# Kernel optimization log

Measured on AMD Instinct MI355X. Metric: run time of the kernel, lower is better.

## Reference

```python
import jax, jax.numpy as jnp
import numpy as np

N_NEWS, N_ENT, N_TOP = 100000, 50000, 2000
D = 128
N_EDGES = 1600000
HID, OUT = 512, 128


def setup_inputs() -> dict:
    key = jax.random.key(0)
    ks = jax.random.split(key, 12)
    return {
        "news_feats": jax.random.normal(ks[0], (N_NEWS, D), jnp.float32),
        "entity_feats": jax.random.normal(ks[1], (N_ENT, D), jnp.float32),
        "topic_feats": jax.random.normal(ks[2], (N_TOP, D), jnp.float32),
        "ent_row": jax.random.randint(ks[3], (N_EDGES,), 0, N_NEWS, jnp.int32),
        "ent_col": jax.random.randint(ks[4], (N_EDGES,), 0, N_ENT, jnp.int32),
        "top_row": jax.random.randint(ks[5], (N_EDGES,), 0, N_NEWS, jnp.int32),
        "top_col": jax.random.randint(ks[6], (N_EDGES,), 0, N_TOP, jnp.int32),
        "W1": jax.random.normal(ks[7], (3 * D, HID), jnp.float32) * 0.05,
        "b1": jnp.zeros((HID,), jnp.float32),
        "W2": jax.random.normal(ks[8], (HID, OUT), jnp.float32) * 0.05,
        "b2": jnp.zeros((OUT,), jnp.float32),
    }


def _agg(feats, row, col, num_news):
    # SpMM with binary adjacency: sum neighbor feats per news node
    gathered = feats[col]                                   # [E, D]
    summed = jax.ops.segment_sum(gathered, row, num_segments=num_news)
    deg = jax.ops.segment_sum(jnp.ones_like(row, dtype=feats.dtype), row,
                              num_segments=num_news)
    return summed / (deg[:, None] + 1e-8)


def reference(news_feats, entity_feats, topic_feats, ent_row, ent_col,
              top_row, top_col, W1, b1, W2, b2):
    n = news_feats.shape[0]
    ent_agg = _agg(entity_feats, ent_row, ent_col, n)
    top_agg = _agg(topic_feats, top_row, top_col, n)
    out = jnp.concatenate([news_feats, ent_agg, top_agg], axis=1)  # [N, 3D]
    h = jnp.tanh(out @ W1 + b1)
    return h @ W2 + b2
```

## Files before the change

### kernel.cpp

```cpp
#include <hip/hip_runtime.h>
#include <hip/hip_bf16.h>

#define NN 100000
#define NE 50000
#define NT 2000
#define DD 128
#define NEDGE 1600000
#define HID 512
#define OUTD 128
#define K1 (3*DD)
#define NBKT 391
#define ECAP 4608

typedef __bf16 bf16x8 __attribute__((ext_vector_type(8)));
typedef __bf16 bf16x4 __attribute__((ext_vector_type(4)));
typedef float  f32x4  __attribute__((ext_vector_type(4)));

__device__ __forceinline__ __bf16 f2b(float f) {
    __hip_bfloat16 h = __float2bfloat16(f);
    union { __hip_bfloat16 h; __bf16 b; } u; u.h = h; return u.b;
}

__device__ __forceinline__ void gll16(const void* g, void* l) {
    __builtin_amdgcn_global_load_lds((const __attribute__((address_space(1))) void*)g,
                                     (__attribute__((address_space(3))) void*)l, 16, 0, 0);
}

__device__ __forceinline__ float ftanh(float x) {
    x = fminf(fmaxf(x, -15.f), 15.f);
    float t = __expf(2.f * x);
    return (t - 1.f) / (t + 1.f);
}

__global__ void conv_feats(const float* __restrict__ entf, const float* __restrict__ topf,
                           const float* __restrict__ news,
                           __bf16* __restrict__ entb, __bf16* __restrict__ topb,
                           __bf16* __restrict__ X) {
    long i = ((long)blockIdx.x * 256 + threadIdx.x) * 4;
    const long NEL = (long)NE * DD;
    const long NTL = (long)NT * DD;
    if (i < NEL) {
        float4 v = *(const float4*)(entf + i);
        *(bf16x4*)(entb + i) = bf16x4{f2b(v.x), f2b(v.y), f2b(v.z), f2b(v.w)};
    } else if (i < NEL + NTL) {
        long j = i - NEL;
        float4 v = *(const float4*)(topf + j);
        *(bf16x4*)(topb + j) = bf16x4{f2b(v.x), f2b(v.y), f2b(v.z), f2b(v.w)};
    } else {
        long j = i - NEL - NTL;
        long row = j >> 7, col = j & 127;
        float4 v = *(const float4*)(news + j);
        *(bf16x4*)(X + row * K1 + col) = bf16x4{f2b(v.x), f2b(v.y), f2b(v.z), f2b(v.w)};
    }
}

__global__ __launch_bounds__(256) void scatter_bucket(const int* __restrict__ er,
                                                      const int* __restrict__ ec,
                                                      const int* __restrict__ tr,
                                                      const int* __restrict__ tc,
                                                      int* __restrict__ cnt_e,
                                                      int* __restrict__ cnt_t,
                                                      int* __restrict__ be,
                                                      int* __restrict__ bt) {
    __shared__ int lhe[NBKT], lht[NBKT];
    __shared__ int lbe[NBKT], lbt[NBKT];
    const int tid = threadIdx.x;
    for (int i = tid; i < NBKT; i += 256) { lhe[i] = 0; lht[i] = 0; }
    __syncthreads();
    const int base = blockIdx.x * 4096;
    #pragma unroll 4
    for (int k = 0; k < 16; k++) {
        int e = base + k * 256 + tid;
        if (e < NEDGE) {
            atomicAdd(&lhe[er[e] >> 8], 1);
            atomicAdd(&lht[tr[e] >> 8], 1);
        }
    }
    __syncthreads();
    for (int i = tid; i < NBKT; i += 256) {
        int c = lhe[i];
        lbe[i] = c ? (i * ECAP + atomicAdd(&cnt_e[i], c)) : 0;
        lhe[i] = 0;
        c = lht[i];
        lbt[i] = c ? (i * ECAP + atomicAdd(&cnt_t[i], c)) : 0;
        lht[i] = 0;
    }
    __syncthreads();
    #pragma unroll 4
    for (int k = 0; k < 16; k++) {
        int e = base + k * 256 + tid;
        if (e < NEDGE) {
            int r = er[e];
            int b = r >> 8;
            int p = lbe[b] + atomicAdd(&lhe[b], 1);
            be[p] = ((r & 255) << 16) | ec[e];
            r = tr[e];
            b = r >> 8;
            p = lbt[b] + atomicAdd(&lht[b], 1);
            bt[p] = ((r & 255) << 16) | tc[e];
        }
    }
}

__global__ __launch_bounds__(256) void bucket_csr(const int* __restrict__ be,
                                                  const int* __restrict__ bt,
                                                  const int* __restrict__ cnt_e,
                                                  const int* __restrict__ cnt_t,
                                                  int* __restrict__ starts_e,
                                                  int* __restrict__ ends_e,
                                                  int* __restrict__ starts_t,
                                                  int* __restrict__ ends_t,
                                                  int* __restrict__ se,
                                                  int* __restrict__ st) {
    const int* buf  = blockIdx.y ? bt : be;
    const int* bcnt = blockIdx.y ? cnt_t : cnt_e;
    int* starts     = blockIdx.y ? starts_t : starts_e;
    int* ends       = blockIdx.y ? ends_t : ends_e;
    int* sout       = blockIdx.y ? st : se;
    const int b = blockIdx.x;
    const int tid = threadIdx.x;
    const int start = b * ECAP;
    int cnt = bcnt[b]; if (cnt > ECAP) cnt = ECAP;

    __shared__ int scn[256];
    __shared__ int lcur[256];
    scn[tid] = 0;
    __syncthreads();
    for (int i = tid; i < cnt; i += 256)
        atomicAdd(&scn[buf[start + i] >> 16], 1);
    __syncthreads();
    #pragma unroll
    for (int off = 1; off < 256; off <<= 1) {
        int v = (tid >= off) ? scn[tid - off] : 0;
        __syncthreads();
        scn[tid] += v;
        __syncthreads();
    }
    const int node = b * 256 + tid;
    const int excl = start + (tid ? scn[tid - 1] : 0);
    if (node < NN) {
        starts[node] = excl;
        ends[node]   = start + scn[tid];
    }
    lcur[tid] = excl;
    __syncthreads();
    for (int i = tid; i < cnt; i += 256) {
        int v = buf[start + i];
        int p = atomicAdd(&lcur[v >> 16], 1);
        sout[p] = v & 0xFFFF;
    }
}

__global__ __launch_bounds__(256) void aggregate2(const __bf16* __restrict__ entb,
                                                  const __bf16* __restrict__ topb,
                                                  const int* __restrict__ starts_e,
                                                  const int* __restrict__ ends_e,
                                                  const int* __restrict__ starts_t,
                                                  const int* __restrict__ ends_t,
                                                  const int* __restrict__ se,
                                                  const int* __restrict__ st,
                                                  __bf16* __restrict__ X) {
    __shared__ int sidx[4][128];
    const int wave = threadIdx.x >> 6, lane = threadIdx.x & 63;
    const int node = blockIdx.x * 4 + wave;
    if (node >= NN) return;
    const int g = lane >> 4;
    const int d = (lane & 15) * 8;

    const int s0 = starts_e[node], s1 = ends_e[node];
    const int t0 = starts_t[node], t1 = ends_t[node];
    const int dege = s1 - s0, degt = t1 - t0;
    const int lim_e = dege < 64 ? dege : 64;
    const int lim_t = degt < 64 ? degt : 64;

    int* my = sidx[wave];
    if (lane < lim_e) my[lane] = se[s0 + lane];
    if (lane < lim_t) my[64 + lane] = st[t0 + lane];

    float ea[8] = {0,0,0,0,0,0,0,0};
    float pa[8] = {0,0,0,0,0,0,0,0};

    const int lim = lim_e > lim_t ? lim_e : lim_t;
    for (int e = g; e < lim; e += 4) {
        if (e < lim_e) {
            bf16x8 v = *(const bf16x8*)(entb + (long)my[e] * DD + d);
            #pragma unroll
            for (int j = 0; j < 8; j++) ea[j] += (float)v[j];
        }
        if (e < lim_t) {
            bf16x8 v = *(const bf16x8*)(topb + (long)my[64 + e] * DD + d);
            #pragma unroll
            for (int j = 0; j < 8; j++) pa[j] += (float)v[j];
        }
    }
    for (int e = 64 + g; e < dege; e += 4) {
        bf16x8 v = *(const bf16x8*)(entb + (long)se[s0 + e] * DD + d);
        #pragma unroll
        for (int j = 0; j < 8; j++) ea[j] += (float)v[j];
    }
    for (int e = 64 + g; e < degt; e += 4) {
        bf16x8 v = *(const bf16x8*)(topb + (long)st[t0 + e] * DD + d);
        #pragma unroll
        for (int j = 0; j < 8; j++) pa[j] += (float)v[j];
    }

    #pragma unroll
    for (int j = 0; j < 8; j++) {
        ea[j] += __shfl_xor(ea[j], 16, 64);
        ea[j] += __shfl_xor(ea[j], 32, 64);
        pa[j] += __shfl_xor(pa[j], 16, 64);
        pa[j] += __shfl_xor(pa[j], 32, 64);
    }

    const float ie = 1.0f / ((float)dege + 1e-8f);
    const float it = 1.0f / ((float)degt + 1e-8f);
    __bf16* xr = X + (long)node * K1;
    if (g == 1) {
        *(bf16x8*)(xr + DD + d) = bf16x8{f2b(ea[0]*ie), f2b(ea[1]*ie), f2b(ea[2]*ie), f2b(ea[3]*ie),
                                         f2b(ea[4]*ie), f2b(ea[5]*ie), f2b(ea[6]*ie), f2b(ea[7]*ie)};
    } else if (g == 2) {
        *(bf16x8*)(xr + 2*DD + d) = bf16x8{f2b(pa[0]*it), f2b(pa[1]*it), f2b(pa[2]*it), f2b(pa[3]*it),
                                           f2b(pa[4]*it), f2b(pa[5]*it), f2b(pa[6]*it), f2b(pa[7]*it)};
    }
}

__global__ void conv_w(const float* __restrict__ W1, const float* __restrict__ W2,
                       __bf16* __restrict__ W1T, __bf16* __restrict__ W2T) {
    int i = blockIdx.x * 256 + threadIdx.x;
    if (i < K1 * HID) {
        int k = i / HID, n = i % HID;
        W1T[n * K1 + k] = f2b(W1[i]);
    } else {
        int j = i - K1 * HID;
        if (j < HID * OUTD) {
            int k = j / OUTD, n = j % OUTD;
            W2T[n * HID + k] = f2b(W2[j]);
        }
    }
}


__device__ __forceinline__ void stage_tile(const __bf16* __restrict__ src, int ldK,
                                           int k0, int row0, int rowmax,
                                           __bf16* lds, int w, int lane) {
    #pragma unroll
    for (int half = 0; half < 2; half++) {
        int ss = w * 64 + half * 256 + lane;
        int r = ss >> 2;
        int sw = (r & 3) ^ ((r >> 2) & 3);
        int c = (ss & 3) ^ sw;
        int gr = row0 + r; if (gr >= rowmax) gr = rowmax - 1;
        gll16(src + (long)gr * ldK + k0 + c * 8,
              lds + (w * 64 + half * 256) * 8);
    }
}

__device__ __forceinline__ bf16x8 frag(const __bf16* lds, int r, int q) {
    int sw = (r & 3) ^ ((r >> 2) & 3);
    return *(const bf16x8*)(lds + (r * 4 + (q ^ sw)) * 8);
}

__device__ __forceinline__ void hs_write(__bf16* Hs, int r, int c, __bf16 v) {
    int ch = c >> 3;
    int pch = ((((ch >> 2) ^ ((r >> 2) & 3)) << 2) | ((ch & 3) ^ (r & 3)));
    Hs[(r * 16 + pch) * 8 + (c & 7)] = v;
}
__device__ __forceinline__ bf16x8 hs_frag(const __bf16* Hs, int r, int kk, int q) {
    int pch = (((kk ^ ((r >> 2) & 3)) << 2) | (q ^ (r & 3)));
    return *(const bf16x8*)(Hs + (r * 16 + pch) * 8);
}

__global__ __launch_bounds__(256, 2) void mlp_fused(const __bf16* __restrict__ X,
                                                    const __bf16* __restrict__ W1T,
                                                    const float* __restrict__ b1,
                                                    const __bf16* __restrict__ W2T,
                                                    const float* __restrict__ b2,
                                                    float* __restrict__ out) {
    __shared__ __bf16 Xs[3][128 * 32];
    __shared__ __bf16 Ws[3][128 * 32];
    __shared__ __bf16 Hs[128 * 128];
    const int bm = blockIdx.x * 128;
    const int t = threadIdx.x;
    const int lane = t & 63;
    const int w = t >> 6;
    const int quad = lane >> 4;
    const int l16 = lane & 15;
    const int wm = w >> 1, wn = w & 1;

    f32x4 oacc[4][4];
    #pragma unroll
    for (int i = 0; i < 4; i++)
        #pragma unroll
        for (int j = 0; j < 4; j++)
            #pragma unroll
            for (int r = 0; r < 4; r++) oacc[i][j][r] = 0.0f;

    stage_tile(X,   K1, 0,  bm, NN,  Xs[0], w, lane);
    stage_tile(W1T, K1, 0,  0,  HID, Ws[0], w, lane);
    stage_tile(X,   K1, 32, bm, NN,  Xs[1], w, lane);
    stage_tile(W1T, K1, 32, 0,  HID, Ws[1], w, lane);

    for (int nc = 0; nc < 4; nc++) {
        f32x4 hacc[4][4];
        #pragma unroll
        for (int i = 0; i < 4; i++)
            #pragma unroll
            for (int j = 0; j < 4; j++)
                #pragma unroll
                for (int r = 0; r < 4; r++) hacc[i][j][r] = 0.0f;

        #pragma unroll
        for (int kt = 0; kt < 12; kt++) {
            const int cb = kt % 3;
            if (kt < 11) asm volatile("s_waitcnt vmcnt(4)" ::: "memory");
            else         asm volatile("s_waitcnt vmcnt(0)" ::: "memory");
            __builtin_amdgcn_s_barrier();
            bf16x8 af[4], bfr[4];
            #pragma unroll
            for (int i = 0; i < 4; i++) {
                af[i]  = frag(Xs[cb], wm * 64 + i * 16 + l16, quad);
                bfr[i] = frag(Ws[cb], wn * 64 + i * 16 + l16, quad);
            }
            if (kt < 10) {
                const int nb = (kt + 2) % 3;
                stage_tile(X,   K1, (kt + 2) * 32, bm,       NN,  Xs[nb], w, lane);
                stage_tile(W1T, K1, (kt + 2) * 32, nc * 128, HID, Ws[nb], w, lane);
            }
            __builtin_amdgcn_s_setprio(1);
            #pragma unroll
            for (int i = 0; i < 4; i++)
                #pragma unroll
                for (int j = 0; j < 4; j++)
                    hacc[i][j] = __builtin_amdgcn_mfma_f32_16x16x32_bf16(af[i], bfr[j], hacc[i][j], 0, 0, 0);
            __builtin_amdgcn_s_setprio(0);
        }
        __syncthreads();

        stage_tile(W2T, HID, nc * 128, 0, OUTD, Ws[2], w, lane);

        #pragma unroll
        for (int j = 0; j < 4; j++) {
            const int col = wn * 64 + j * 16 + l16;
            const float bb = b1[nc * 128 + col];
            #pragma unroll
            for (int i = 0; i < 4; i++) {
                const int rbase = wm * 64 + i * 16 + quad * 4;
                #pragma unroll
                for (int r = 0; r < 4; r++)
                    hs_write(Hs, rbase + r, col, f2b(ftanh(hacc[i][j][r] + bb)));
            }
        }
        __syncthreads();

        for (int kk = 0; kk < 4; kk++) {
            __bf16* curb = (kk & 1) ? Xs[2] : Ws[2];
            __bf16* nxtb = (kk & 1) ? Ws[2] : Xs[2];
            if (kk < 3)
                stage_tile(W2T, HID, nc * 128 + (kk + 1) * 32, 0, OUTD, nxtb, w, lane);
            if (nc < 3) {
                if (kk == 2) {
                    stage_tile(X,   K1, 0, bm,             NN,  Xs[0], w, lane);
                    stage_tile(W1T, K1, 0, (nc + 1) * 128, HID, Ws[0], w, lane);
                } else if (kk == 3) {
                    stage_tile(X,   K1, 32, bm,             NN,  Xs[1], w, lane);
                    stage_tile(W1T, K1, 32, (nc + 1) * 128, HID, Ws[1], w, lane);
                }
            }
            bf16x8 af[4], bfr[4];
            #pragma unroll
            for (int i = 0; i < 4; i++) {
                af[i]  = hs_frag(Hs, wm * 64 + i * 16 + l16, kk, quad);
                bfr[i] = frag(curb, wn * 64 + i * 16 + l16, quad);
            }
            __builtin_amdgcn_s_setprio(1);
            #pragma unroll
            for (int i = 0; i < 4; i++)
                #pragma unroll
                for (int j = 0; j < 4; j++)
                    oacc[i][j] = __builtin_amdgcn_mfma_f32_16x16x32_bf16(af[i], bfr[j], oacc[i][j], 0, 0, 0);
            __builtin_amdgcn_s_setprio(0);
            __syncthreads();
        }
    }

    float bb[4];
    #pragma unroll
    for (int j = 0; j < 4; j++) bb[j] = b2[wn * 64 + j * 16 + l16];
    #pragma unroll
    for (int i = 0; i < 4; i++) {
        #pragma unroll
        for (int r = 0; r < 4; r++) {
            const int gr = bm + wm * 64 + i * 16 + quad * 4 + r;
            if (gr < NN) {
                float* orow = out + (long)gr * OUTD + wn * 64 + l16;
                #pragma unroll
                for (int j = 0; j < 4; j++)
                    orow[j * 16] = oacc[i][j][r] + bb[j];
            }
        }
    }
}

extern "C" void kernel_launch(void* const* d_in, const int* in_sizes, int n_in,
                              void* d_out, int out_size, void* d_ws, size_t ws_size,
                              hipStream_t stream) {
    const float* news  = (const float*)d_in[0];
    const float* ent_f = (const float*)d_in[1];
    const float* top_f = (const float*)d_in[2];
    const int* ent_row = (const int*)d_in[3];
    const int* ent_col = (const int*)d_in[4];
    const int* top_row = (const int*)d_in[5];
    const int* top_col = (const int*)d_in[6];
    const float* W1 = (const float*)d_in[7];
    const float* b1 = (const float*)d_in[8];
    const float* W2 = (const float*)d_in[9];
    const float* b2 = (const float*)d_in[10];

    char* ws = (char*)d_ws;
    int* starts_e = (int*)(ws + 0);
    int* ends_e   = (int*)(ws + 400016);
    int* starts_t = (int*)(ws + 800032);
    int* ends_t   = (int*)(ws + 1200048);
    int* cnt_e    = (int*)(ws + 1600064);
    int* cnt_t    = (int*)(ws + 1601664);
    __bf16* entb = (__bf16*)(ws + 26406336);
    __bf16* topb = (__bf16*)(ws + 39206336);
    int* be      = (int*)(ws + 40000000);
    int* bt      = (int*)(ws + 48000000);
    int* se      = (int*)(ws + 56000000);
    int* st      = (int*)(ws + 64000000);
    __bf16* X   = (__bf16*)(ws + 102400000);
    __bf16* W1T = (__bf16*)(ws + 179200000);
    __bf16* W2T = (__bf16*)(ws + 179593216);

    hipMemsetAsync(ws + 1600064, 0, 3200, stream);
    conv_w<<<1024, 256, 0, stream>>>(W1, W2, W1T, W2T);
    conv_feats<<<19000, 256, 0, stream>>>(ent_f, top_f, news, entb, topb, X);
    scatter_bucket<<<392, 256, 0, stream>>>(ent_row, ent_col, top_row, top_col,
                                            cnt_e, cnt_t, be, bt);
    bucket_csr<<<dim3(NBKT, 2), 256, 0, stream>>>(be, bt, cnt_e, cnt_t,
                                                  starts_e, ends_e, starts_t, ends_t,
                                                  se, st);
    aggregate2<<<NN / 4, 256, 0, stream>>>(entb, topb, starts_e, ends_e,
                                           starts_t, ends_t, se, st, X);
    mlp_fused<<<782, 256, 0, stream>>>(X, W1T, b1, W2T, b2, (float*)d_out);
}
```

Before: 488.9 us.

## Fuse preprocessing kernels and merge bucket CSR build with aggregation in LDS

Merges the weight conversion, feature conversion and edge bucketing kernels into one `prep` launch that picks its role from the block index. Merges per-bucket CSR construction with neighbour aggregation into `csr_agg`. It keeps the sorted column indices and per-node offsets in shared memory, so the global starts/ends/sorted-index arrays and their round trip are gone. The goal is fewer kernel launches and less global memory traffic. The trade-off is that aggregation now runs on only 391 blocks of 8 waves, each walking 32 nodes in sequence. That leaves far fewer waves to hide gather latency than the previous one-wave-per-node launch.

```diff
diff --git a/kernel.cpp b/kernel.cpp
--- a/kernel.cpp
+++ b/kernel.cpp
@@ -11,6 +11,9 @@
 #define K1 (3*DD)
 #define NBKT 391
 #define ECAP 4608
+#define CFB 19000
+#define SCB 392
+#define CWB 1024
 
 typedef __bf16 bf16x8 __attribute__((ext_vector_type(8)));
 typedef __bf16 bf16x4 __attribute__((ext_vector_type(4)));
@@ -32,209 +35,213 @@
     return (t - 1.f) / (t + 1.f);
 }
 
-__global__ void conv_feats(const float* __restrict__ entf, const float* __restrict__ topf,
-                           const float* __restrict__ news,
-                           __bf16* __restrict__ entb, __bf16* __restrict__ topb,
-                           __bf16* __restrict__ X) {
-    long i = ((long)blockIdx.x * 256 + threadIdx.x) * 4;
-    const long NEL = (long)NE * DD;
-    const long NTL = (long)NT * DD;
-    if (i < NEL) {
-        float4 v = *(const float4*)(entf + i);
-        *(bf16x4*)(entb + i) = bf16x4{f2b(v.x), f2b(v.y), f2b(v.z), f2b(v.w)};
-    } else if (i < NEL + NTL) {
-        long j = i - NEL;
-        float4 v = *(const float4*)(topf + j);
-        *(bf16x4*)(topb + j) = bf16x4{f2b(v.x), f2b(v.y), f2b(v.z), f2b(v.w)};
-    } else {
-        long j = i - NEL - NTL;
-        long row = j >> 7, col = j & 127;
-        float4 v = *(const float4*)(news + j);
-        *(bf16x4*)(X + row * K1 + col) = bf16x4{f2b(v.x), f2b(v.y), f2b(v.z), f2b(v.w)};
-    }
-}
-
-__global__ __launch_bounds__(256) void scatter_bucket(const int* __restrict__ er,
-                                                      const int* __restrict__ ec,
-                                                      const int* __restrict__ tr,
-                                                      const int* __restrict__ tc,
-                                                      int* __restrict__ cnt_e,
-                                                      int* __restrict__ cnt_t,
-                                                      int* __restrict__ be,
-                                                      int* __restrict__ bt) {
+__global__ __launch_bounds__(256) void prep(const float* __restrict__ entf,
+                                            const float* __restrict__ topf,
+                                            const float* __restrict__ news,
+                                            const int* __restrict__ er,
+                                            const int* __restrict__ ec,
+                                            const int* __restrict__ tr,
+                                            const int* __restrict__ tc,
+                                            const float* __restrict__ W1,
+                                            const float* __restrict__ W2,
+                                            __bf16* __restrict__ entb,
+                                            __bf16* __restrict__ topb,
+                                            __bf16* __restrict__ X,
+                                            int* __restrict__ cnt_e,
+                                            int* __restrict__ cnt_t,
+                                            int* __restrict__ be,
+                                            int* __restrict__ bt,
+                                            __bf16* __restrict__ W1T,
+                                            __bf16* __restrict__ W2T) {
     __shared__ int lhe[NBKT], lht[NBKT];
     __shared__ int lbe[NBKT], lbt[NBKT];
+    const int bx = blockIdx.x;
     const int tid = threadIdx.x;
-    for (int i = tid; i < NBKT; i += 256) { lhe[i] = 0; lht[i] = 0; }
-    __syncthreads();
-    const int base = blockIdx.x * 4096;
-    #pragma unroll 4
-    for (int k = 0; k < 16; k++) {
-        int e = base + k * 256 + tid;
-        if (e < NEDGE) {
-            atomicAdd(&lhe[er[e] >> 8], 1);
-            atomicAdd(&lht[tr[e] >> 8], 1);
-        }
-    }
-    __syncthreads();
-    for (int i = tid; i < NBKT; i += 256) {
-        int c = lhe[i];
-        lbe[i] = c ? (i * ECAP + atomicAdd(&cnt_e[i], c)) : 0;
-        lhe[i] = 0;
-        c = lht[i];
-        lbt[i] = c ? (i * ECAP + atomicAdd(&cnt_t[i], c)) : 0;
-        lht[i] = 0;
-    }
-    __syncthreads();
-    #pragma unroll 4
-    for (int k = 0; k < 16; k++) {
-        int e = base + k * 256 + tid;
-        if (e < NEDGE) {
-            int r = er[e];
-            int b = r >> 8;
-            int p = lbe[b] + atomicAdd(&lhe[b], 1);
-            be[p] = ((r & 255) << 16) | ec[e];
-            r = tr[e];
-            b = r >> 8;
-            p = lbt[b] + atomicAdd(&lht[b], 1);
-            bt[p] = ((r & 255) << 16) | tc[e];
-        }
-    }
-}
-
-__global__ __launch_bounds__(256) void bucket_csr(const int* __restrict__ be,
-                                                  const int* __restrict__ bt,
-                                                  const int* __restrict__ cnt_e,
-                                                  const int* __restrict__ cnt_t,
-                                                  int* __restrict__ starts_e,
-                                                  int* __restrict__ ends_e,
-                                                  int* __restrict__ starts_t,
-                                                  int* __restrict__ ends_t,
-                                                  int* __restrict__ se,
-                                                  int* __restrict__ st) {
-    const int* buf  = blockIdx.y ? bt : be;
-    const int* bcnt = blockIdx.y ? cnt_t : cnt_e;
-    int* starts     = blockIdx.y ? starts_t : starts_e;
-    int* ends       = blockIdx.y ? ends_t : ends_e;
-    int* sout       = blockIdx.y ? st : se;
+
+    if (bx < CFB) {
+        long i = ((long)bx * 256 + tid) * 4;
+        const long NEL = (long)NE * DD;
+        const long NTL = (long)NT * DD;
+        if (i < NEL) {
+            float4 v = *(const float4*)(entf + i);
+            *(bf16x4*)(entb + i) = bf16x4{f2b(v.x), f2b(v.y), f2b(v.z), f2b(v.w)};
+        } else if (i < NEL + NTL) {
+            long j = i - NEL;
+            float4 v = *(const float4*)(topf + j);
+            *(bf16x4*)(topb + j) = bf16x4{f2b(v.x), f2b(v.y), f2b(v.z), f2b(v.w)};
+        } else {
+            long j = i - NEL - NTL;
+            long row = j >> 7, col = j & 127;
+            float4 v = *(const float4*)(news + j);
+            *(bf16x4*)(X + row * K1 + col) = bf16x4{f2b(v.x), f2b(v.y), f2b(v.z), f2b(v.w)};
+        }
+    } else if (bx < CFB + SCB) {
+        const int sb = bx - CFB;
+        for (int i = tid; i < NBKT; i += 256) { lhe[i] = 0; lht[i] = 0; }
+        __syncthreads();
+        const int base = sb * 4096;
+        #pragma unroll 4
+        for (int k = 0; k < 16; k++) {
+            int e = base + k * 256 + tid;
+            if (e < NEDGE) {
+                atomicAdd(&lhe[er[e] >> 8], 1);
+                atomicAdd(&lht[tr[e] >> 8], 1);
+            }
+        }
+        __syncthreads();
+        for (int i = tid; i < NBKT; i += 256) {
+            int c = lhe[i];
+            lbe[i] = c ? (i * ECAP + atomicAdd(&cnt_e[i], c)) : 0;
+            lhe[i] = 0;
+            c = lht[i];
+            lbt[i] = c ? (i * ECAP + atomicAdd(&cnt_t[i], c)) : 0;
+            lht[i] = 0;
+        }
+        __syncthreads();
+        #pragma unroll 4
+        for (int k = 0; k < 16; k++) {
+            int e = base + k * 256 + tid;
+            if (e < NEDGE) {
+                int r = er[e];
+                int b = r >> 8;
+                int p = lbe[b] + atomicAdd(&lhe[b], 1);
+                be[p] = ((r & 255) << 16) | ec[e];
+                r = tr[e];
+                b = r >> 8;
+                p = lbt[b] + atomicAdd(&lht[b], 1);
+                bt[p] = ((r & 255) << 16) | tc[e];
+            }
+        }
+    } else {
+        int i = (bx - CFB - SCB) * 256 + tid;
+        if (i < K1 * HID) {
+            int k = i / HID, n = i % HID;
+            W1T[n * K1 + k] = f2b(W1[i]);
+        } else {
+            int j = i - K1 * HID;
+            if (j < HID * OUTD) {
+                int k = j / OUTD, n = j % OUTD;
+                W2T[n * HID + k] = f2b(W2[j]);
+            }
+        }
+    }
+}
+
+__global__ __launch_bounds__(512) void csr_agg(const int* __restrict__ be,
+                                               const int* __restrict__ bt,
+                                               const int* __restrict__ cnt_e,
+                                               const int* __restrict__ cnt_t,
+                                               const __bf16* __restrict__ entb,
+                                               const __bf16* __restrict__ topb,
+                                               __bf16* __restrict__ X) {
+    __shared__ int lse[ECAP];
+    __shared__ int lst[ECAP];
+    __shared__ int scn[256], lcur[256];
+    __shared__ int nre[256], nrt[256];
     const int b = blockIdx.x;
     const int tid = threadIdx.x;
-    const int start = b * ECAP;
-    int cnt = bcnt[b]; if (cnt > ECAP) cnt = ECAP;
-
-    __shared__ int scn[256];
-    __shared__ int lcur[256];
-    scn[tid] = 0;
+    const int base = b * ECAP;
+
+    {
+        int cnt = cnt_e[b]; if (cnt > ECAP) cnt = ECAP;
+        if (tid < 256) scn[tid] = 0;
+        __syncthreads();
+        for (int i = tid; i < cnt; i += 512)
+            atomicAdd(&scn[be[base + i] >> 16], 1);
+        __syncthreads();
+        #pragma unroll
+        for (int off = 1; off < 256; off <<= 1) {
+            int v = 0;
+            if (tid < 256 && tid >= off) v = scn[tid - off];
+            __syncthreads();
+            if (tid < 256) scn[tid] += v;
+            __syncthreads();
+        }
+        if (tid < 256) {
+            int excl = tid ? scn[tid - 1] : 0;
+            nre[tid] = (excl << 16) | (scn[tid] - excl);
+            lcur[tid] = excl;
+        }
+        __syncthreads();
+        for (int i = tid; i < cnt; i += 512) {
+            int v = be[base + i];
+            int p = atomicAdd(&lcur[v >> 16], 1);
+            lse[p] = v & 0xFFFF;
+        }
+    }
     __syncthreads();
-    for (int i = tid; i < cnt; i += 256)
-        atomicAdd(&scn[buf[start + i] >> 16], 1);
+    {
+        int cnt = cnt_t[b]; if (cnt > ECAP) cnt = ECAP;
+        if (tid < 256) scn[tid] = 0;
+        __syncthreads();
+        for (int i = tid; i < cnt; i += 512)
+            atomicAdd(&scn[bt[base + i] >> 16], 1);
+        __syncthreads();
+        #pragma unroll
+        for (int off = 1; off < 256; off <<= 1) {
+            int v = 0;
+            if (tid < 256 && tid >= off) v = scn[tid - off];
+            __syncthreads();
+            if (tid < 256) scn[tid] += v;
+            __syncthreads();
+        }
+        if (tid < 256) {
+            int excl = tid ? scn[tid - 1] : 0;
+            nrt[tid] = (excl << 16) | (scn[tid] - excl);
+            lcur[tid] = excl;
+        }
+        __syncthreads();
+        for (int i = tid; i < cnt; i += 512) {
+            int v = bt[base + i];
+            int p = atomicAdd(&lcur[v >> 16], 1);
+            lst[p] = v & 0xFFFF;
+        }
+    }
     __syncthreads();
-    #pragma unroll
-    for (int off = 1; off < 256; off <<= 1) {
-        int v = (tid >= off) ? scn[tid - off] : 0;
-        __syncthreads();
-        scn[tid] += v;
-        __syncthreads();
-    }
-    const int node = b * 256 + tid;
-    const int excl = start + (tid ? scn[tid - 1] : 0);
-    if (node < NN) {
-        starts[node] = excl;
-        ends[node]   = start + scn[tid];
-    }
-    lcur[tid] = excl;
-    __syncthreads();
-    for (int i = tid; i < cnt; i += 256) {
-        int v = buf[start + i];
-        int p = atomicAdd(&lcur[v >> 16], 1);
-        sout[p] = v & 0xFFFF;
-    }
-}
-
-__global__ __launch_bounds__(256) void aggregate2(const __bf16* __restrict__ entb,
-                                                  const __bf16* __restrict__ topb,
-                                                  const int* __restrict__ starts_e,
-                                                  const int* __restrict__ ends_e,
-                                                  const int* __restrict__ starts_t,
-                                                  const int* __restrict__ ends_t,
-                                                  const int* __restrict__ se,
-                                                  const int* __restrict__ st,
-                                                  __bf16* __restrict__ X) {
-    __shared__ int sidx[4][128];
-    const int wave = threadIdx.x >> 6, lane = threadIdx.x & 63;
-    const int node = blockIdx.x * 4 + wave;
-    if (node >= NN) return;
+
+    const int wave = tid >> 6, lane = tid & 63;
     const int g = lane >> 4;
     const int d = (lane & 15) * 8;
-
-    const int s0 = starts_e[node], s1 = ends_e[node];
-    const int t0 = starts_t[node], t1 = ends_t[node];
-    const int dege = s1 - s0, degt = t1 - t0;
-    const int lim_e = dege < 64 ? dege : 64;
-    const int lim_t = degt < 64 ? degt : 64;
-
-    int* my = sidx[wave];
-    if (lane < lim_e) my[lane] = se[s0 + lane];
-    if (lane < lim_t) my[64 + lane] = st[t0 + lane];
-
-    float ea[8] = {0,0,0,0,0,0,0,0};
-    float pa[8] = {0,0,0,0,0,0,0,0};
-
-    const int lim = lim_e > lim_t ? lim_e : lim_t;
-    for (int e = g; e < lim; e += 4) {
-        if (e < lim_e) {
-            bf16x8 v = *(const bf16x8*)(entb + (long)my[e] * DD + d);
-            #pragma unroll
-            for (int j = 0; j < 8; j++) ea[j] += (float)v[j];
-        }
-        if (e < lim_t) {
-            bf16x8 v = *(const bf16x8*)(topb + (long)my[64 + e] * DD + d);
-            #pragma unroll
-            for (int j = 0; j < 8; j++) pa[j] += (float)v[j];
-        }
-    }
-    for (int e = 64 + g; e < dege; e += 4) {
-        bf16x8 v = *(const bf16x8*)(entb + (long)se[s0 + e] * DD + d);
-        #pragma unroll
-        for (int j = 0; j < 8; j++) ea[j] += (float)v[j];
-    }
-    for (int e = 64 + g; e < degt; e += 4) {
-        bf16x8 v = *(const bf16x8*)(topb + (long)st[t0 + e] * DD + d);
-        #pragma unroll
-        for (int j = 0; j < 8; j++) pa[j] += (float)v[j];
-    }
-
-    #pragma unroll
-    for (int j = 0; j < 8; j++) {
-        ea[j] += __shfl_xor(ea[j], 16, 64);
-        ea[j] += __shfl_xor(ea[j], 32, 64);
-        pa[j] += __shfl_xor(pa[j], 16, 64);
-        pa[j] += __shfl_xor(pa[j], 32, 64);
-    }
-
-    const float ie = 1.0f / ((float)dege + 1e-8f);
-    const float it = 1.0f / ((float)degt + 1e-8f);
-    __bf16* xr = X + (long)node * K1;
-    if (g == 1) {
-        *(bf16x8*)(xr + DD + d) = bf16x8{f2b(ea[0]*ie), f2b(ea[1]*ie), f2b(ea[2]*ie), f2b(ea[3]*ie),
-                                         f2b(ea[4]*ie), f2b(ea[5]*ie), f2b(ea[6]*ie), f2b(ea[7]*ie)};
-    } else if (g == 2) {
-        *(bf16x8*)(xr + 2*DD + d) = bf16x8{f2b(pa[0]*it), f2b(pa[1]*it), f2b(pa[2]*it), f2b(pa[3]*it),
-                                           f2b(pa[4]*it), f2b(pa[5]*it), f2b(pa[6]*it), f2b(pa[7]*it)};
-    }
-}
-
-__global__ void conv_w(const float* __restrict__ W1, const float* __restrict__ W2,
-                       __bf16* __restrict__ W1T, __bf16* __restrict__ W2T) {
-    int i = blockIdx.x * 256 + threadIdx.x;
-    if (i < K1 * HID) {
-        int k = i / HID, n = i % HID;
-        W1T[n * K1 + k] = f2b(W1[i]);
-    } else {
-        int j = i - K1 * HID;
-        if (j < HID * OUTD) {
-            int k = j / OUTD, n = j % OUTD;
-            W2T[n * HID + k] = f2b(W2[j]);
+    for (int ln = wave; ln < 256; ln += 8) {
+        const int node = b * 256 + ln;
+        if (node >= NN) break;
+        const int pe = nre[ln], pt = nrt[ln];
+        const int e0 = pe >> 16, dege = pe & 0xFFFF;
+        const int t0 = pt >> 16, degt = pt & 0xFFFF;
+
+        float ea[8] = {0,0,0,0,0,0,0,0};
+        float pa[8] = {0,0,0,0,0,0,0,0};
+        const int lim = dege > degt ? dege : degt;
+        for (int e = g; e < lim; e += 4) {
+            if (e < dege) {
+                bf16x8 v = *(const bf16x8*)(entb + (long)lse[e0 + e] * DD + d);
+                #pragma unroll
+                for (int j = 0; j < 8; j++) ea[j] += (float)v[j];
+            }
+            if (e < degt) {
+                bf16x8 v = *(const bf16x8*)(topb + (long)lst[t0 + e] * DD + d);
+                #pragma unroll
+                for (int j = 0; j < 8; j++) pa[j] += (float)v[j];
+            }
+        }
+
+        #pragma unroll
+        for (int j = 0; j < 8; j++) {
+            ea[j] += __shfl_xor(ea[j], 16, 64);
+            ea[j] += __shfl_xor(ea[j], 32, 64);
+            pa[j] += __shfl_xor(pa[j], 16, 64);
+            pa[j] += __shfl_xor(pa[j], 32, 64);
+        }
+
+        const float ie = 1.0f / ((float)dege + 1e-8f);
+        const float it = 1.0f / ((float)degt + 1e-8f);
+        __bf16* xr = X + (long)node * K1;
+        if (g == 1) {
+            *(bf16x8*)(xr + DD + d) = bf16x8{f2b(ea[0]*ie), f2b(ea[1]*ie), f2b(ea[2]*ie), f2b(ea[3]*ie),
+                                             f2b(ea[4]*ie), f2b(ea[5]*ie), f2b(ea[6]*ie), f2b(ea[7]*ie)};
+        } else if (g == 2) {
+            *(bf16x8*)(xr + 2*DD + d) = bf16x8{f2b(pa[0]*it), f2b(pa[1]*it), f2b(pa[2]*it), f2b(pa[3]*it),
+                                               f2b(pa[4]*it), f2b(pa[5]*it), f2b(pa[6]*it), f2b(pa[7]*it)};
         }
     }
 }
@@ -417,31 +424,21 @@
     const float* b2 = (const float*)d_in[10];
 
     char* ws = (char*)d_ws;
-    int* starts_e = (int*)(ws + 0);
-    int* ends_e   = (int*)(ws + 400016);
-    int* starts_t = (int*)(ws + 800032);
-    int* ends_t   = (int*)(ws + 1200048);
     int* cnt_e    = (int*)(ws + 1600064);
     int* cnt_t    = (int*)(ws + 1601664);
     __bf16* entb = (__bf16*)(ws + 26406336);
     __bf16* topb = (__bf16*)(ws + 39206336);
     int* be      = (int*)(ws + 40000000);
     int* bt      = (int*)(ws + 48000000);
-    int* se      = (int*)(ws + 56000000);
-    int* st      = (int*)(ws + 64000000);
     __bf16* X   = (__bf16*)(ws + 102400000);
     __bf16* W1T = (__bf16*)(ws + 179200000);
     __bf16* W2T = (__bf16*)(ws + 179593216);
 
     hipMemsetAsync(ws + 1600064, 0, 3200, stream);
-    conv_w<<<1024, 256, 0, stream>>>(W1, W2, W1T, W2T);
-    conv_feats<<<19000, 256, 0, stream>>>(ent_f, top_f, news, entb, topb, X);
-    scatter_bucket<<<392, 256, 0, stream>>>(ent_row, ent_col, top_row, top_col,
-                                            cnt_e, cnt_t, be, bt);
-    bucket_csr<<<dim3(NBKT, 2), 256, 0, stream>>>(be, bt, cnt_e, cnt_t,
-                                                  starts_e, ends_e, starts_t, ends_t,
-                                                  se, st);
-    aggregate2<<<NN / 4, 256, 0, stream>>>(entb, topb, starts_e, ends_e,
-                                           starts_t, ends_t, se, st, X);
+    prep<<<CFB + SCB + CWB, 256, 0, stream>>>(ent_f, top_f, news,
+                                              ent_row, ent_col, top_row, top_col,
+                                              W1, W2, entb, topb, X,
+                                              cnt_e, cnt_t, be, bt, W1T, W2T);
+    csr_agg<<<NBKT, 512, 0, stream>>>(be, bt, cnt_e, cnt_t, entb, topb, X);
     mlp_fused<<<782, 256, 0, stream>>>(X, W1T, b1, W2T, b2, (float*)d_out);
 }
```

Result: slower. 580.7 us (+18.8%).
